# Optimization experiments

Hardware: AMD Instinct MI355X
Metric: run time of the kernel (lower is better)

The kernel has to match this reference:

```python
import jax, jax.numpy as jnp
import numpy as np
import math

B = 2        # batch
S = 4095     # input sequence (cls token makes L = 4096)
F_IN = 32    # input feature size
D = 512      # d_model (hidden_size)
H = 8        # n_heads
E = D // H   # head dim = 64
DFF = 2048   # feedforward dim
NL = 2       # encoder layers
FACTOR = 5   # probsparse sampling factor
EPS = 1e-5


def setup_inputs() -> dict:
    key = jax.random.key(0)
    ks = jax.random.split(key, 16)

    def w(k, shape):
        return jax.random.normal(k, shape, dtype=jnp.float32) * 0.02

    inp = {}
    inp['x'] = jax.random.normal(ks[0], (B, S, F_IN), dtype=jnp.float32)
    inp['We'] = w(ks[1], (D, F_IN)); inp['be'] = jnp.zeros((D,), jnp.float32)
    inp['cls'] = jnp.zeros((1, 1, D), jnp.float32)
    inp['Wq'] = w(ks[2], (NL, D, D)); inp['bq'] = jnp.zeros((NL, D), jnp.float32)
    inp['Wk'] = w(ks[3], (NL, D, D)); inp['bk'] = jnp.zeros((NL, D), jnp.float32)
    inp['Wv'] = w(ks[4], (NL, D, D)); inp['bv'] = jnp.zeros((NL, D), jnp.float32)
    inp['Wo'] = w(ks[5], (NL, D, D)); inp['bo'] = jnp.zeros((NL, D), jnp.float32)
    inp['g1'] = jnp.ones((NL, D), jnp.float32); inp['b1'] = jnp.zeros((NL, D), jnp.float32)
    inp['g2'] = jnp.ones((NL, D), jnp.float32); inp['b2'] = jnp.zeros((NL, D), jnp.float32)
    inp['W1'] = w(ks[6], (NL, DFF, D)); inp['bf1'] = jnp.zeros((NL, DFF), jnp.float32)
    inp['W2'] = w(ks[7], (NL, D, DFF)); inp['bf2'] = jnp.zeros((NL, D), jnp.float32)
    inp['Wf'] = w(ks[8], (1, D)); inp['bf'] = jnp.zeros((1,), jnp.float32)
    return inp


def pos_encoding(L):
    # Sinusoidal positional encoding [L, D]
    pos = jnp.arange(L, dtype=jnp.float32)[:, None]
    div = jnp.exp(jnp.arange(0, D, 2, dtype=jnp.float32) * (-math.log(10000.0) / D))
    pe = jnp.zeros((L, D), jnp.float32)
    pe = pe.at[:, 0::2].set(jnp.sin(pos * div))
    pe = pe.at[:, 1::2].set(jnp.cos(pos * div))
    return pe


def layer_norm(x, g, b):
    mu = x.mean(-1, keepdims=True)
    var = ((x - mu) ** 2).mean(-1, keepdims=True)
    return (x - mu) / jnp.sqrt(var + EPS) * g + b


def prob_attention(q, k, v, rng):
    # q, k, v: [B, H, L, E]; mask_flag=False (encoder self-attention)
    b, h, L, e = q.shape
    u = min(FACTOR * int(np.ceil(np.log(L))), L)  # sample_k == n_top here (L_Q == L_K)
    idx = jax.random.randint(rng, (L, u), 0, L)   # random K sampling per query position
    Ks = k[:, :, idx, :]                          # [B,H,L,u,E] gather
    QKs = jnp.einsum('bhle,bhlue->bhlu', q, Ks)   # sampled scores
    M = QKs.max(-1) - QKs.sum(-1) / L             # sparsity measure [B,H,L]
    _, top = jax.lax.top_k(M, u)                  # active query indices [B,H,u]
    Qr = jnp.take_along_axis(q, top[..., None], axis=2)      # [B,H,u,E]
    scores = jnp.einsum('bhue,bhke->bhuk', Qr, k) / math.sqrt(e)
    attn = jax.nn.softmax(scores, axis=-1)
    ctx = jnp.broadcast_to(v.mean(axis=2, keepdims=True), (b, h, L, e))  # initial context = mean(V)
    upd = jnp.einsum('bhuk,bhke->bhue', attn, v)
    bi = jnp.arange(b)[:, None, None]
    hi = jnp.arange(h)[None, :, None]
    ctx = ctx.at[bi, hi, top].set(upd)            # scatter active-query contexts
    return ctx                                    # [B,H,L,E]


def attention_layer(x, Wq_, bq_, Wk_, bk_, Wv_, bv_, Wo_, bo_, rng):
    b, L, _ = x.shape
    q = (x @ Wq_.T + bq_).reshape(b, L, H, E).transpose(0, 2, 1, 3)
    k = (x @ Wk_.T + bk_).reshape(b, L, H, E).transpose(0, 2, 1, 3)
    v = (x @ Wv_.T + bv_).reshape(b, L, H, E).transpose(0, 2, 1, 3)
    ctx = prob_attention(q, k, v, rng)            # [B,H,L,E]
    out = ctx.transpose(0, 2, 1, 3).reshape(b, L, D)
    return out @ Wo_.T + bo_


def reference(x, We, be, cls, Wq, bq, Wk, bk, Wv, bv, Wo, bo, g1, b1, g2, b2, W1, bf1, W2, bf2, Wf, bf):
    h = x @ We.T + be                                            # [B,S,D]
    h = jnp.concatenate([jnp.broadcast_to(cls, (B, 1, D)), h], axis=1)  # prepend cls
    L = h.shape[1]
    h = h + pos_encoding(L)[None]
    for l in range(NL):
        rng = jax.random.fold_in(jax.random.key(42), l)
        a = attention_layer(h, Wq[l], bq[l], Wk[l], bk[l], Wv[l], bv[l], Wo[l], bo[l], rng)
        h = layer_norm(h + a, g1[l], b1[l])
        y = jax.nn.relu(h @ W1[l].T + bf1[l])
        y = y @ W2[l].T + bf2[l]
        h = layer_norm(h + y, g2[l], b2[l])
    return h[:, 0] @ Wf.T + bf  # cls-token prediction head [B,1]
```

## Files before the change

kernel.cpp:

```cpp
#include <hip/hip_runtime.h>
#include <hip/hip_bf16.h>
#include <math.h>
#include <stdint.h>

#define B 2
#define S 4095
#define LSEQ 4096
#define F_IN 32
#define D 512
#define H 8
#define E 64
#define DFF 2048
#define NL 2
#define U 45
#define EPSL 1e-5f
#define LU (LSEQ * U)
#define HALF_LU (LU / 2)
#define NS 32
#define SLICE 128

typedef __attribute__((ext_vector_type(8))) short short8;
typedef __attribute__((ext_vector_type(4))) float f32x4;

#define GLD(gp, lp)                                                            \
    __builtin_amdgcn_global_load_lds(                                          \
        (const __attribute__((address_space(1))) void*)(gp),                   \
        (__attribute__((address_space(3))) void*)(lp), 16, 0, 0)

__device__ __forceinline__ unsigned short bf16_bits(float f) {
    __hip_bfloat16 h = __float2bfloat16(f);
    return *(unsigned short*)&h;
}
__device__ __forceinline__ float bits_to_f32(unsigned short s) {
    union { uint32_t u; float f; } c;
    c.u = ((uint32_t)s) << 16;
    return c.f;
}
__device__ __forceinline__ unsigned long long mkey(float v, int index) {
    uint32_t u = __float_as_uint(v);
    uint32_t mono = (u & 0x80000000u) ? ~u : (u | 0x80000000u);
    return ((unsigned long long)mono << 32) | (uint32_t)(0xFFFFFFFFu - (uint32_t)index);
}

__device__ __forceinline__ uint32_t rotl32(uint32_t x, int r) {
    return (x << r) | (x >> (32 - r));
}

__device__ void threefry2x32(uint32_t k0, uint32_t k1, uint32_t c0, uint32_t c1,
                             uint32_t& o0, uint32_t& o1) {
    uint32_t ks2 = k0 ^ k1 ^ 0x1BD11BDAu;
    uint32_t x0 = c0 + k0, x1 = c1 + k1;
    x0 += x1; x1 = rotl32(x1, 13); x1 ^= x0;
    x0 += x1; x1 = rotl32(x1, 15); x1 ^= x0;
    x0 += x1; x1 = rotl32(x1, 26); x1 ^= x0;
    x0 += x1; x1 = rotl32(x1, 6);  x1 ^= x0;
    x0 += k1; x1 += ks2 + 1u;
    x0 += x1; x1 = rotl32(x1, 17); x1 ^= x0;
    x0 += x1; x1 = rotl32(x1, 29); x1 ^= x0;
    x0 += x1; x1 = rotl32(x1, 16); x1 ^= x0;
    x0 += x1; x1 = rotl32(x1, 24); x1 ^= x0;
    x0 += ks2; x1 += k0 + 2u;
    x0 += x1; x1 = rotl32(x1, 13); x1 ^= x0;
    x0 += x1; x1 = rotl32(x1, 15); x1 ^= x0;
    x0 += x1; x1 = rotl32(x1, 26); x1 ^= x0;
    x0 += x1; x1 = rotl32(x1, 6);  x1 ^= x0;
    x0 += k0; x1 += k1 + 3u;
    x0 += x1; x1 = rotl32(x1, 17); x1 ^= x0;
    x0 += x1; x1 = rotl32(x1, 29); x1 ^= x0;
    x0 += x1; x1 = rotl32(x1, 16); x1 ^= x0;
    x0 += x1; x1 = rotl32(x1, 24); x1 ^= x0;
    x0 += k1; x1 += ks2 + 4u;
    x0 += x1; x1 = rotl32(x1, 13); x1 ^= x0;
    x0 += x1; x1 = rotl32(x1, 15); x1 ^= x0;
    x0 += x1; x1 = rotl32(x1, 26); x1 ^= x0;
    x0 += x1; x1 = rotl32(x1, 6);  x1 ^= x0;
    x0 += ks2; x1 += k0 + 5u;
    o0 = x0; o1 = x1;
}

__global__ void idx_kernel(int* __restrict__ idx, int layer) {
    int j = blockIdx.x * blockDim.x + threadIdx.x;
    if (j >= HALF_LU) return;
    uint32_t f0, f1, a0, a1, b0, b1, o0, o1;
    threefry2x32(0u, 42u, 0u, (uint32_t)layer, f0, f1);
    threefry2x32(f0, f1, 0u, 2u, a0, a1);
    threefry2x32(f0, f1, 1u, 3u, b0, b1);
    threefry2x32(a1, b1, (uint32_t)j, (uint32_t)(j + HALF_LU), o0, o1);
    idx[j] = (int)(o0 & 4095u);
    idx[j + HALF_LU] = (int)(o1 & 4095u);
    (void)a0; (void)b0;
}

__global__ void prep_embed_kernel(const float* __restrict__ x, const float* __restrict__ We,
                                  __hip_bfloat16* __restrict__ xbf,
                                  __hip_bfloat16* __restrict__ webf) {
    int u = blockIdx.x * blockDim.x + threadIdx.x;
    const int NX = B * LSEQ * F_IN / 4;
    const int NW = D * F_IN / 4;
    if (u < NX) {
        int e0 = u * 4;
        int i = e0 & 31;
        int l = (e0 >> 5) & (LSEQ - 1);
        int b = e0 >> 17;
        union { unsigned short s[4]; uint2 w; } o;
        if (l == 0) {
            o.s[0] = o.s[1] = o.s[2] = o.s[3] = 0;
        } else {
            float4 v = *(const float4*)(x + ((size_t)b * S + (l - 1)) * F_IN + i);
            o.s[0] = bf16_bits(v.x); o.s[1] = bf16_bits(v.y);
            o.s[2] = bf16_bits(v.z); o.s[3] = bf16_bits(v.w);
        }
        ((uint2*)xbf)[u] = o.w;
    } else if (u < NX + NW) {
        int w = u - NX;
        float4 v = ((const float4*)We)[w];
        union { unsigned short s[4]; uint2 w2; } o;
        o.s[0] = bf16_bits(v.x); o.s[1] = bf16_bits(v.y);
        o.s[2] = bf16_bits(v.z); o.s[3] = bf16_bits(v.w);
        ((uint2*)webf)[w] = o.w2;
    }
}

__global__ void posenc_kernel(const float* __restrict__ emb, const float* __restrict__ cls,
                              float* __restrict__ h, __hip_bfloat16* __restrict__ hbf) {
    int gid = blockIdx.x * blockDim.x + threadIdx.x;
    if (gid >= B * LSEQ * D) return;
    int d = gid % D;
    int l = (gid / D) % LSEQ;
    float v = (l == 0) ? cls[d] : emb[gid];
    int i = d >> 1;
    float divv = expf((float)(2 * i) * (float)(-9.210340371976184 / 512.0));
    float ang = (float)l * divv;
    v += (d & 1) ? cosf(ang) : sinf(ang);
    h[gid] = v;
    hbf[gid] = __float2bfloat16(v);
}

__global__ void cast_weights_kernel(const float* __restrict__ Wq_l,
                                    const float* __restrict__ Wk_l,
                                    const float* __restrict__ Wv_l,
                                    const float* __restrict__ Wo_l,
                                    const float* __restrict__ W1_l,
                                    const float* __restrict__ W2_l,
                                    const float* __restrict__ bq_l,
                                    const float* __restrict__ bk_l,
                                    const float* __restrict__ bv_l,
                                    __hip_bfloat16* __restrict__ wqb,
                                    __hip_bfloat16* __restrict__ wkb,
                                    __hip_bfloat16* __restrict__ wvb,
                                    __hip_bfloat16* __restrict__ wob,
                                    __hip_bfloat16* __restrict__ w1b,
                                    __hip_bfloat16* __restrict__ w2b,
                                    float* __restrict__ qkvbias) {
    const int SDD = D * D / 4;
    const int SFD = DFF * D / 4;
    const int CAST_N = 4 * SDD + 2 * SFD;
    int u = blockIdx.x * blockDim.x + threadIdx.x;
    if (u >= CAST_N) {
        int j = u - CAST_N;
        if (j < 384) {
            int seg = (j * 4) >> 9;
            int off = (j * 4) & 511;
            const float* src = (seg == 0) ? bq_l : (seg == 1) ? bk_l : bv_l;
            *(float4*)(qkvbias + j * 4) = *(const float4*)(src + off);
        }
        return;
    }
    const float* src;
    __hip_bfloat16* dst;
    int off;
    if (u < SDD) { src = Wq_l; dst = wqb; off = u; }
    else if (u < 2 * SDD) { src = Wk_l; dst = wkb; off = u - SDD; }
    else if (u < 3 * SDD) { src = Wv_l; dst = wvb; off = u - 2 * SDD; }
    else if (u < 4 * SDD) { src = Wo_l; dst = wob; off = u - 3 * SDD; }
    else if (u < 4 * SDD + SFD) { src = W1_l; dst = w1b; off = u - 4 * SDD; }
    else { src = W2_l; dst = w2b; off = u - 4 * SDD - SFD; }
    float4 v = ((const float4*)src)[off];
    union { unsigned short s[4]; uint2 w; } o;
    o.s[0] = bf16_bits(v.x); o.s[1] = bf16_bits(v.y);
    o.s[2] = bf16_bits(v.z); o.s[3] = bf16_bits(v.w);
    ((uint2*)dst)[off] = o.w;
}

__global__ __launch_bounds__(256) void gemm32(const unsigned short* __restrict__ A,
                                              const unsigned short* __restrict__ W,
                                              const float* __restrict__ bias,
                                              float* __restrict__ Cf,
                                              int M, int N, int K) {
    __shared__ unsigned short lds[2 * 128 * 32];
    unsigned short* As = lds;
    unsigned short* Bs = lds + 128 * 32;
    const int tid = threadIdx.x;
    const int m0 = blockIdx.y * 128, n0 = blockIdx.x * 128;
    const int wave = tid >> 6, lane = tid & 63;
    const int wm = (wave >> 1) * 64, wn = (wave & 1) * 64;
    const int quad = lane >> 4, m15 = lane & 15;
    const int srow = tid >> 2, scol = (tid & 3) * 8;
    f32x4 acc[4][4] = {};
    const unsigned short* Ag0 = A + (size_t)(m0 + srow) * K + scol;
    const unsigned short* Ag1 = A + (size_t)(m0 + srow + 64) * K + scol;
    const unsigned short* Wg0 = W + (size_t)(n0 + srow) * K + scol;
    const unsigned short* Wg1 = W + (size_t)(n0 + srow + 64) * K + scol;
    for (int k0 = 0; k0 < K; k0 += 32) {
        __syncthreads();
        GLD(Ag0 + k0, As + tid * 8);
        GLD(Ag1 + k0, As + 2048 + tid * 8);
        GLD(Wg0 + k0, Bs + tid * 8);
        GLD(Wg1 + k0, Bs + 2048 + tid * 8);
        __syncthreads();
        short8 af[4], bfr[4];
#pragma unroll
        for (int mi = 0; mi < 4; ++mi)
            af[mi] = *(const short8*)(As + (wm + mi * 16 + m15) * 32 + quad * 8);
#pragma unroll
        for (int ni = 0; ni < 4; ++ni)
            bfr[ni] = *(const short8*)(Bs + (wn + ni * 16 + m15) * 32 + quad * 8);
#pragma unroll
        for (int mi = 0; mi < 4; ++mi)
#pragma unroll
            for (int ni = 0; ni < 4; ++ni)
                acc[mi][ni] = __builtin_amdgcn_mfma_f32_16x16x32_bf16(
                    af[mi], bfr[ni], acc[mi][ni], 0, 0, 0);
    }
#pragma unroll
    for (int mi = 0; mi < 4; ++mi) {
        int mg = m0 + wm + mi * 16 + quad * 4;
#pragma unroll
        for (int ni = 0; ni < 4; ++ni) {
            int ng = n0 + wn + ni * 16 + m15;
            float bv = bias[ng];
#pragma unroll
            for (int r = 0; r < 4; ++r)
                Cf[(size_t)(mg + r) * N + ng] = acc[mi][ni][r] + bv;
        }
    }
}

template <int MODE>
__global__ __launch_bounds__(256) void gemm_pipe(const unsigned short* __restrict__ A,
                                                 const unsigned short* __restrict__ W,
                                                 const float* __restrict__ bias,
                                                 void* __restrict__ C0,
                                                 void* __restrict__ C1,
                                                 void* __restrict__ C2,
                                                 int M, int N, int K, int NBN) {
    __shared__ unsigned short As[2][128 * 32];
    __shared__ unsigned short Bs[2][128 * 32];
    const int tid = threadIdx.x;
    const int NBM = M >> 7;
    const int bid = blockIdx.x;
    const int xcd = bid & 7, local = bid >> 3;
    const int m_t = xcd * (NBM >> 3) + local / NBN;
    const int n_t = local % NBN;
    const int m0 = m_t * 128, n0 = n_t * 128;
    const int wave = tid >> 6, lane = tid & 63;
    const int wm = (wave >> 1) * 64, wn = (wave & 1) * 64;
    const int quad = lane >> 4, m15 = lane & 15;
    const int srow = tid >> 2, scol = (tid & 3) * 8;
    f32x4 acc[4][4] = {};
    const unsigned short* Ag0 = A + (size_t)(m0 + srow) * K + scol;
    const unsigned short* Ag1 = A + (size_t)(m0 + srow + 64) * K + scol;
    const unsigned short* Wg0 = W + (size_t)(n0 + srow) * K + scol;
    const unsigned short* Wg1 = W + (size_t)(n0 + srow + 64) * K + scol;
    GLD(Ag0, As[0] + tid * 8);
    GLD(Ag1, As[0] + 2048 + tid * 8);
    GLD(Wg0, Bs[0] + tid * 8);
    GLD(Wg1, Bs[0] + 2048 + tid * 8);
    int cur = 0;
    for (int k0 = 0; k0 < K; k0 += 32) {
        __syncthreads();
        int kn = k0 + 32;
        if (kn < K) {
            GLD(Ag0 + kn, As[cur ^ 1] + tid * 8);
            GLD(Ag1 + kn, As[cur ^ 1] + 2048 + tid * 8);
            GLD(Wg0 + kn, Bs[cur ^ 1] + tid * 8);
            GLD(Wg1 + kn, Bs[cur ^ 1] + 2048 + tid * 8);
        }
        short8 af[4], bfr[4];
#pragma unroll
        for (int mi = 0; mi < 4; ++mi)
            af[mi] = *(const short8*)(As[cur] + (wm + mi * 16 + m15) * 32 + quad * 8);
#pragma unroll
        for (int ni = 0; ni < 4; ++ni)
            bfr[ni] = *(const short8*)(Bs[cur] + (wn + ni * 16 + m15) * 32 + quad * 8);
#pragma unroll
        for (int mi = 0; mi < 4; ++mi)
#pragma unroll
            for (int ni = 0; ni < 4; ++ni)
                acc[mi][ni] = __builtin_amdgcn_mfma_f32_16x16x32_bf16(
                    af[mi], bfr[ni], acc[mi][ni], 0, 0, 0);
        cur ^= 1;
    }
#pragma unroll
    for (int mi = 0; mi < 4; ++mi) {
        int mg = m0 + wm + mi * 16 + quad * 4;
#pragma unroll
        for (int ni = 0; ni < 4; ++ni) {
            int ng = n0 + wn + ni * 16 + m15;
            float bv = bias[ng];
#pragma unroll
            for (int r = 0; r < 4; ++r) {
                float v = acc[mi][ni][r] + bv;
                if (MODE == 0) {
                    ((float*)C0)[(size_t)(mg + r) * N + ng] = v;
                } else if (MODE == 1) {
                    ((__hip_bfloat16*)C0)[(size_t)(mg + r) * N + ng] = __float2bfloat16(v);
                } else if (MODE == 2) {
                    ((__hip_bfloat16*)C0)[(size_t)(mg + r) * N + ng] =
                        __float2bfloat16(fmaxf(v, 0.f));
                } else {
                    int seg = ng >> 9;
                    int col = ng & 511;
                    if (seg == 0)
                        ((float*)C0)[(size_t)(mg + r) * D + col] = v;
                    else if (seg == 1)
                        ((__hip_bfloat16*)C1)[(size_t)(mg + r) * D + col] = __float2bfloat16(v);
                    else
                        ((__hip_bfloat16*)C2)[(size_t)(mg + r) * D + col] = __float2bfloat16(v);
                }
            }
        }
    }
}

__global__ __launch_bounds__(256) void gemm64_m64(const unsigned short* __restrict__ A,
                                                  const unsigned short* __restrict__ W,
                                                  const float* __restrict__ bias,
                                                  float* __restrict__ Cf,
                                                  int M, int N, int K, int NBN) {
    __shared__ unsigned short As[2][64 * 32];
    __shared__ unsigned short Bs[2][128 * 32];
    const int tid = threadIdx.x;
    const int NBM = M >> 6;
    const int bid = blockIdx.x;
    const int xcd = bid & 7, local = bid >> 3;
    const int m_t = xcd * (NBM >> 3) + local / NBN;
    const int n_t = local % NBN;
    const int m0 = m_t * 64, n0 = n_t * 128;
    const int wave = tid >> 6, lane = tid & 63;
    const int quad = lane >> 4, m15 = lane & 15;
    const int srow = tid >> 2, scol = (tid & 3) * 8;
    f32x4 acc[8] = {};
    const unsigned short* Ag0 = A + (size_t)(m0 + srow) * K + scol;
    const unsigned short* Wg0 = W + (size_t)(n0 + srow) * K + scol;
    const unsigned short* Wg1 = W + (size_t)(n0 + srow + 64) * K + scol;
    for (int k0 = 0; k0 < K; k0 += 64) {
        __syncthreads();
        if (tid * 8 < 64 * 32) {
            GLD(Ag0 + k0, As[0] + tid * 8);
            GLD(Ag0 + k0 + 32, As[1] + tid * 8);
        }
        GLD(Wg0 + k0, Bs[0] + tid * 8);
        GLD(Wg1 + k0, Bs[0] + 2048 + tid * 8);
        GLD(Wg0 + k0 + 32, Bs[1] + tid * 8);
        GLD(Wg1 + k0 + 32, Bs[1] + 2048 + tid * 8);
        __syncthreads();
#pragma unroll
        for (int ks = 0; ks < 2; ++ks) {
            short8 af = *(const short8*)(As[ks] + (wave * 16 + m15) * 32 + quad * 8);
#pragma unroll
            for (int ni = 0; ni < 8; ++ni) {
                short8 bfr = *(const short8*)(Bs[ks] + (ni * 16 + m15) * 32 + quad * 8);
                acc[ni] = __builtin_amdgcn_mfma_f32_16x16x32_bf16(af, bfr, acc[ni], 0, 0, 0);
            }
        }
    }
    int mg = m0 + wave * 16 + quad * 4;
#pragma unroll
    for (int ni = 0; ni < 8; ++ni) {
        int ng = n0 + ni * 16 + m15;
        float bv = bias[ng];
#pragma unroll
        for (int r = 0; r < 4; ++r)
            Cf[(size_t)(mg + r) * N + ng] = acc[ni][r] + bv;
    }
}

__global__ __launch_bounds__(256) void mscore_kernel(const float* __restrict__ q,
                                                     const __hip_bfloat16* __restrict__ kbf,
                                                     const int* __restrict__ idx,
                                                     float* __restrict__ Mv) {
    __shared__ float Sbuf[U][8];
    __shared__ int sidx[U];
    int bid = blockIdx.x;
    int b = bid & 1;
    int l = bid >> 1;
    int tid = threadIdx.x;
    int wave = tid >> 6, lane = tid & 63;
    if (tid < U) sidx[tid] = idx[l * U + tid];
    const float* qr = q + ((size_t)(b * LSEQ) + l) * D + lane * 8;
    float4 qa = *(const float4*)qr;
    float4 qb = *(const float4*)(qr + 4);
    __syncthreads();
    const unsigned short* kbase = (const unsigned short*)(kbf + (size_t)(b * LSEQ) * D);
    for (int t = wave; t < U; t += 4) {
        int kr = sidx[t];
        union { uint4 u; unsigned short s[8]; } kv;
        kv.u = *(const uint4*)(kbase + (size_t)kr * D + lane * 8);
        float p = qa.x * bits_to_f32(kv.s[0]) + qa.y * bits_to_f32(kv.s[1]) +
                  qa.z * bits_to_f32(kv.s[2]) + qa.w * bits_to_f32(kv.s[3]) +
                  qb.x * bits_to_f32(kv.s[4]) + qb.y * bits_to_f32(kv.s[5]) +
                  qb.z * bits_to_f32(kv.s[6]) + qb.w * bits_to_f32(kv.s[7]);
        p += __shfl_xor(p, 1);
        p += __shfl_xor(p, 2);
        p += __shfl_xor(p, 4);
        if ((lane & 7) == 0) Sbuf[t][lane >> 3] = p;
    }
    __syncthreads();
    if (tid < 8) {
        float mx = -INFINITY, sm = 0.f;
        for (int t = 0; t < U; ++t) {
            float v = Sbuf[t][tid];
            mx = fmaxf(mx, v);
            sm += v;
        }
        Mv[((size_t)b * H + tid) * LSEQ + l] = mx - sm / (float)LSEQ;
    }
}

__global__ __launch_bounds__(256) void topk_chunk_kernel(const float* __restrict__ Mv,
                                                         unsigned long long* __restrict__ cand) {
    __shared__ unsigned long long sk[256];
    int blk = blockIdx.x;
    int chunk = blk & 15, bh = blk >> 4;
    int tid = threadIdx.x;
    int gi = chunk * 256 + tid;
    sk[tid] = mkey(Mv[(size_t)bh * LSEQ + gi], gi);
    __syncthreads();
    for (int k = 2; k <= 256; k <<= 1) {
        for (int j = k >> 1; j > 0; j >>= 1) {
            int ixj = tid ^ j;
            if (ixj > tid) {
                unsigned long long a = sk[tid], b = sk[ixj];
                bool desc = ((tid & k) == 0);
                if (desc ? (a < b) : (a > b)) { sk[tid] = b; sk[ixj] = a; }
            }
            __syncthreads();
        }
    }
    if (tid < U) cand[((size_t)bh * 16 + chunk) * U + tid] = sk[tid];
}

__global__ __launch_bounds__(256) void topk_merge_kernel(const unsigned long long* __restrict__ cand,
                                                         int* __restrict__ top) {
    __shared__ unsigned long long sk[1024];
    int bh = blockIdx.x;
    int tid = threadIdx.x;
    for (int e = tid; e < 1024; e += 256)
        sk[e] = (e < 16 * U) ? cand[(size_t)bh * 16 * U + e] : 0ull;
    __syncthreads();
    for (int k = 2; k <= 1024; k <<= 1) {
        for (int j = k >> 1; j > 0; j >>= 1) {
            for (int e = tid; e < 1024; e += 256) {
                int ixj = e ^ j;
                if (ixj > e) {
                    unsigned long long a = sk[e], b = sk[ixj];
                    bool desc = ((e & k) == 0);
                    if (desc ? (a < b) : (a > b)) { sk[e] = b; sk[ixj] = a; }
                }
            }
            __syncthreads();
        }
    }
    if (tid < U)
        top[bh * U + tid] = (int)(0xFFFFFFFFu - (uint32_t)(sk[tid] & 0xFFFFFFFFu));
}

__global__ __launch_bounds__(256) void vmean_part(const __hip_bfloat16* __restrict__ v,
                                                  float* __restrict__ part) {
    int blk = blockIdx.x;
    int seg = blk & 7, hh = (blk >> 3) & 7, b = blk >> 6;
    int e = threadIdx.x & 63, rg = threadIdx.x >> 6;
    const __hip_bfloat16* vp =
        v + ((size_t)(b * LSEQ) + seg * 512) * D + hh * 64 + e;
    float acc = 0.f;
    for (int r = rg; r < 512; r += 4) acc += __bfloat162float(vp[(size_t)r * D]);
    __shared__ float red[4][64];
    red[rg][e] = acc;
    __syncthreads();
    if (threadIdx.x < 64)
        part[(size_t)blk * 64 + threadIdx.x] =
            red[0][threadIdx.x] + red[1][threadIdx.x] + red[2][threadIdx.x] + red[3][threadIdx.x];
}

__global__ void vmean_reduce(const float* __restrict__ part, float* __restrict__ vm) {
    int gid = blockIdx.x * blockDim.x + threadIdx.x;
    if (gid >= B * H * E) return;
    int e = gid & 63, bh = gid >> 6;
    float acc = 0.f;
#pragma unroll
    for (int s = 0; s < 8; ++s) acc += part[((size_t)bh * 8 + s) * 64 + e];
    vm[gid] = acc / (float)LSEQ;
}

__global__ __launch_bounds__(256) void wo_base_kernel(const float* __restrict__ vm,
                                                      const unsigned short* __restrict__ wob,
                                                      const float* __restrict__ bo,
                                                      float* __restrict__ base) {
    int b = blockIdx.x >> 7;
    int n = (blockIdx.x & 127) * 4 + (threadIdx.x >> 6);
    int lane = threadIdx.x & 63;
    const float* vmr = vm + (size_t)b * D + lane * 8;
    float4 va = *(const float4*)vmr;
    float4 vb = *(const float4*)(vmr + 4);
    union { uint4 u; unsigned short s[8]; } w;
    w.u = *(const uint4*)(wob + (size_t)n * D + lane * 8);
    float p = va.x * bits_to_f32(w.s[0]) + va.y * bits_to_f32(w.s[1]) +
              va.z * bits_to_f32(w.s[2]) + va.w * bits_to_f32(w.s[3]) +
              vb.x * bits_to_f32(w.s[4]) + vb.y * bits_to_f32(w.s[5]) +
              vb.z * bits_to_f32(w.s[6]) + vb.w * bits_to_f32(w.s[7]);
    for (int off = 32; off; off >>= 1) p += __shfl_xor(p, off);
    if (lane == 0) base[(size_t)b * D + n] = p + bo[n];
}

__global__ void bcast_base(const float* __restrict__ base, float* __restrict__ aout) {
    int i = blockIdx.x * blockDim.x + threadIdx.x;
    if (i >= B * LSEQ * D / 4) return;
    int b = i >> 19;
    int c4 = i & 127;
    ((float4*)aout)[i] = *(const float4*)(base + (size_t)b * D + c4 * 4);
}

__global__ __launch_bounds__(256) void wo_corr_kernel(const float* __restrict__ updbuf,
                                                      const float* __restrict__ vm,
                                                      const unsigned short* __restrict__ wob,
                                                      const int* __restrict__ top,
                                                      float* __restrict__ aout) {
    __shared__ float dlt[E];
    int bid = blockIdx.x;
    int t = bid % U;
    int bh = bid / U;
    int b = bh >> 3, hh = bh & 7;
    int tid = threadIdx.x;
    if (tid < E) dlt[tid] = updbuf[((size_t)bh * U + t) * E + tid] - vm[(size_t)bh * E + tid];
    __syncthreads();
    int r = top[bh * U + t];
    float* arow = aout + (size_t)(b * LSEQ + r) * D;
    for (int n = tid; n < D; n += 256) {
        const unsigned short* wr = wob + (size_t)n * D + hh * E;
        float acc = 0.f;
#pragma unroll
        for (int k2 = 0; k2 < E; ++k2) acc += dlt[k2] * bits_to_f32(wr[k2]);
        atomicAdd(arow + n, acc);
    }
}

__global__ __launch_bounds__(256) void attn_part(const float* __restrict__ q,
                                                 const __hip_bfloat16* __restrict__ kbf,
                                                 const __hip_bfloat16* __restrict__ vbf,
                                                 const int* __restrict__ top,
                                                 float* __restrict__ Opart,
                                                 float* __restrict__ msum) {
    __shared__ unsigned short Qs[48 * 72];
    __shared__ unsigned short Ks[SLICE * 72];
    __shared__ unsigned short Vs[SLICE * 68];
    __shared__ unsigned short Ps[48 * 136];
    __shared__ float mred[48][4];
    __shared__ float sred[48][4];
    const int slice = blockIdx.x, hh = blockIdx.y, b = blockIdx.z;
    const int bh = b * H + hh;
    const int tid = threadIdx.x;
    const int s0 = slice * SLICE;
    for (int i = tid; i < 48 * 64; i += 256) {
        int t = i >> 6, e = i & 63;
        float v = 0.f;
        if (t < U) {
            int r = top[bh * U + t];
            v = q[((size_t)(b * LSEQ) + r) * D + hh * E + e];
        }
        Qs[t * 72 + e] = bf16_bits(v);
    }
    {
        const uint4* src = (const uint4*)(kbf + ((size_t)(b * LSEQ) + s0) * D + hh * E);
        for (int i = tid; i < SLICE * 8; i += 256) {
            int r = i >> 3, c = i & 7;
            uint4 d = src[(size_t)r * 64 + c];
            *(uint4*)(Ks + r * 72 + c * 8) = d;
        }
    }
    {
        const uint2* src = (const uint2*)(vbf + ((size_t)(b * LSEQ) + s0) * D + hh * E);
        for (int i = tid; i < SLICE * 16; i += 256) {
            int r = i >> 4, c = i & 15;
            uint2 d = src[(size_t)r * 128 + c];
            *(uint2*)(Vs + r * 68 + c * 4) = d;
        }
    }
    __syncthreads();
    const int wave = tid >> 6, lane = tid & 63;
    const int quad = lane >> 4, m15 = lane & 15;
    const int wc = wave * 32;
    f32x4 acc[3][2] = {};
#pragma unroll
    for (int ks = 0; ks < 2; ++ks) {
        short8 af[3], bfr[2];
#pragma unroll
        for (int mt = 0; mt < 3; ++mt)
            af[mt] = *(const short8*)(Qs + (mt * 16 + m15) * 72 + ks * 32 + quad * 8);
#pragma unroll
        for (int nt = 0; nt < 2; ++nt)
            bfr[nt] = *(const short8*)(Ks + (wc + nt * 16 + m15) * 72 + ks * 32 + quad * 8);
#pragma unroll
        for (int mt = 0; mt < 3; ++mt)
#pragma unroll
            for (int nt = 0; nt < 2; ++nt)
                acc[mt][nt] = __builtin_amdgcn_mfma_f32_16x16x32_bf16(
                    af[mt], bfr[nt], acc[mt][nt], 0, 0, 0);
    }
    float sc[3][2][4];
#pragma unroll
    for (int mt = 0; mt < 3; ++mt)
#pragma unroll
        for (int nt = 0; nt < 2; ++nt)
#pragma unroll
            for (int r = 0; r < 4; ++r) sc[mt][nt][r] = acc[mt][nt][r] * 0.125f;
#pragma unroll
    for (int mt = 0; mt < 3; ++mt)
#pragma unroll
        for (int r = 0; r < 4; ++r) {
            float mv = fmaxf(sc[mt][0][r], sc[mt][1][r]);
            mv = fmaxf(mv, __shfl_xor(mv, 1));
            mv = fmaxf(mv, __shfl_xor(mv, 2));
            mv = fmaxf(mv, __shfl_xor(mv, 4));
            mv = fmaxf(mv, __shfl_xor(mv, 8));
            if (m15 == 0) mred[mt * 16 + quad * 4 + r][wave] = mv;
        }
    __syncthreads();
#pragma unroll
    for (int mt = 0; mt < 3; ++mt)
#pragma unroll
        for (int r = 0; r < 4; ++r) {
            int row = mt * 16 + quad * 4 + r;
            float ms = fmaxf(fmaxf(mred[row][0], mred[row][1]),
                             fmaxf(mred[row][2], mred[row][3]));
            float p0 = __expf(sc[mt][0][r] - ms);
            float p1 = __expf(sc[mt][1][r] - ms);
            float sv = p0 + p1;
            sv += __shfl_xor(sv, 1);
            sv += __shfl_xor(sv, 2);
            sv += __shfl_xor(sv, 4);
            sv += __shfl_xor(sv, 8);
            if (m15 == 0) sred[row][wave] = sv;
            Ps[row * 136 + wc + m15] = bf16_bits(p0);
            Ps[row * 136 + wc + 16 + m15] = bf16_bits(p1);
        }
    __syncthreads();
    if (tid < U) {
        float mm = fmaxf(fmaxf(mred[tid][0], mred[tid][1]),
                         fmaxf(mred[tid][2], mred[tid][3]));
        float ss = sred[tid][0] + sred[tid][1] + sred[tid][2] + sred[tid][3];
        size_t base = (((size_t)bh * NS + slice) * U + tid) * 2;
        msum[base] = mm;
        msum[base + 1] = ss;
    }
    f32x4 apv[3] = {};
#pragma unroll
    for (int ks = 0; ks < 4; ++ks) {
        short8 bv;
#pragma unroll
        for (int j = 0; j < 8; ++j)
            bv[j] = (short)Vs[(ks * 32 + quad * 8 + j) * 68 + wave * 16 + m15];
        short8 af2[3];
#pragma unroll
        for (int mt = 0; mt < 3; ++mt)
            af2[mt] = *(const short8*)(Ps + (mt * 16 + m15) * 136 + ks * 32 + quad * 8);
#pragma unroll
        for (int mt = 0; mt < 3; ++mt)
            apv[mt] = __builtin_amdgcn_mfma_f32_16x16x32_bf16(af2[mt], bv, apv[mt], 0, 0, 0);
    }
    size_t obase = ((size_t)bh * NS + slice) * U;
#pragma unroll
    for (int mt = 0; mt < 3; ++mt)
#pragma unroll
        for (int r = 0; r < 4; ++r) {
            int row = mt * 16 + quad * 4 + r;
            if (row < U)
                Opart[(obase + row) * 64 + wave * 16 + m15] = apv[mt][r];
        }
}

__global__ __launch_bounds__(64) void attn_reduce(const float* __restrict__ Opart,
                                                  const float* __restrict__ msum,
                                                  float* __restrict__ updbuf) {
    int t = blockIdx.x % U;
    int bh = blockIdx.x / U;
    int lane = threadIdx.x;
    float m_s = -INFINITY, ss = 0.f;
    if (lane < NS) {
        size_t base = (((size_t)bh * NS + lane) * U + t) * 2;
        m_s = msum[base];
        ss = msum[base + 1];
    }
    float M = m_s;
    for (int off = 32; off; off >>= 1) M = fmaxf(M, __shfl_xor(M, off));
    float e_s = (lane < NS) ? __expf(m_s - M) : 0.f;
    float d = ss * e_s;
    for (int off = 32; off; off >>= 1) d += __shfl_xor(d, off);
    float acc = 0.f;
    for (int s = 0; s < NS; ++s) {
        float w = __shfl(e_s, s);
        acc += w * Opart[(((size_t)bh * NS + s) * U + t) * 64 + lane];
    }
    updbuf[((size_t)bh * U + t) * E + lane] = acc / d;
}

__global__ __launch_bounds__(64) void add_ln_kernel(float* __restrict__ h,
                                                    const float* __restrict__ a,
                                                    const float* __restrict__ g,
                                                    const float* __restrict__ bb,
                                                    __hip_bfloat16* __restrict__ hbf) {
    int row = blockIdx.x;
    int lane = threadIdx.x;
    float* hp = h + (size_t)row * D;
    const float* ap = a + (size_t)row * D;
    float x[8];
    float sum = 0.f;
#pragma unroll
    for (int j = 0; j < 8; ++j) {
        x[j] = hp[lane + 64 * j] + ap[lane + 64 * j];
        sum += x[j];
    }
    for (int off = 32; off; off >>= 1) sum += __shfl_xor(sum, off);
    float mu = sum / (float)D;
    float vs = 0.f;
#pragma unroll
    for (int j = 0; j < 8; ++j) {
        float dd = x[j] - mu;
        vs += dd * dd;
    }
    for (int off = 32; off; off >>= 1) vs += __shfl_xor(vs, off);
    float inv = 1.f / sqrtf(vs / (float)D + EPSL);
#pragma unroll
    for (int j = 0; j < 8; ++j) {
        float o = (x[j] - mu) * inv * g[lane + 64 * j] + bb[lane + 64 * j];
        hp[lane + 64 * j] = o;
        hbf[(size_t)row * D + lane + 64 * j] = __float2bfloat16(o);
    }
}

__global__ void final_kernel(const float* __restrict__ h, const float* __restrict__ Wf,
                             const float* __restrict__ bf, float* __restrict__ out) {
    int b = blockIdx.x;
    int lane = threadIdx.x;
    const float* hp = h + (size_t)b * LSEQ * D;
    float acc = 0.f;
    for (int j = lane; j < D; j += 64) acc += hp[j] * Wf[j];
    for (int off = 32; off; off >>= 1) acc += __shfl_xor(acc, off);
    if (lane == 0) out[b] = acc + bf[0];
}

extern "C" void kernel_launch(void* const* d_in, const int* in_sizes, int n_in,
                              void* d_out, int out_size, void* d_ws, size_t ws_size,
                              hipStream_t stream) {
    (void)in_sizes; (void)n_in; (void)out_size; (void)ws_size;
    const float* x   = (const float*)d_in[0];
    const float* We  = (const float*)d_in[1];
    const float* be  = (const float*)d_in[2];
    const float* cls = (const float*)d_in[3];
    const float* Wq  = (const float*)d_in[4];
    const float* bq  = (const float*)d_in[5];
    const float* Wk  = (const float*)d_in[6];
    const float* bk  = (const float*)d_in[7];
    const float* Wv  = (const float*)d_in[8];
    const float* bv  = (const float*)d_in[9];
    const float* Wo  = (const float*)d_in[10];
    const float* bo  = (const float*)d_in[11];
    const float* g1  = (const float*)d_in[12];
    const float* b1  = (const float*)d_in[13];
    const float* g2  = (const float*)d_in[14];
    const float* b2  = (const float*)d_in[15];
    const float* W1  = (const float*)d_in[16];
    const float* bf1 = (const float*)d_in[17];
    const float* W2  = (const float*)d_in[18];
    const float* bf2 = (const float*)d_in[19];
    const float* Wf  = (const float*)d_in[20];
    const float* bff = (const float*)d_in[21];
    float* out = (float*)d_out;

    float* ws = (float*)d_ws;
    const size_t NT = (size_t)B * LSEQ * D;
    float* h    = ws;
    float* aout = ws + NT;
    float* q    = ws + 2 * NT;
    __hip_bfloat16* kbf    = (__hip_bfloat16*)(ws + NT);
    __hip_bfloat16* y1_bf  = (__hip_bfloat16*)(ws + 2 * NT);
    __hip_bfloat16* v_bf   = (__hip_bfloat16*)(ws + 4 * NT);
    __hip_bfloat16* h_bf   = (__hip_bfloat16*)(ws + 5 * NT);
    float* Opart = ws + 3 * NT;
    float* msumb = Opart + (size_t)B * H * NS * U * 64;
    float* wpool = ws + 5 * NT + NT / 2;
    __hip_bfloat16* wqb = (__hip_bfloat16*)wpool;
    __hip_bfloat16* wkb = wqb + (size_t)D * D;
    __hip_bfloat16* wvb = wkb + (size_t)D * D;
    __hip_bfloat16* wob = wvb + (size_t)D * D;
    __hip_bfloat16* w1b = wob + (size_t)D * D;
    __hip_bfloat16* w2b = w1b + (size_t)DFF * D;
    float* after_w = wpool + ((size_t)4 * D * D + 2 * (size_t)DFF * D) / 2;
    float* Mbuf = after_w;
    int* idx    = (int*)(Mbuf + (size_t)B * H * LSEQ);
    int* top    = idx + LU;
    float* vm   = (float*)(top + B * H * U);
    float* vpart  = vm + (size_t)B * H * E;
    float* updbuf = vpart + (size_t)128 * 64;
    float* baseb  = updbuf + (size_t)B * H * U * 64;
    __hip_bfloat16* xbf  = (__hip_bfloat16*)(baseb + (size_t)B * D);
    __hip_bfloat16* webf = xbf + (size_t)B * LSEQ * F_IN;
    unsigned long long* cand =
        (unsigned long long*)(((uintptr_t)(webf + (size_t)D * F_IN) + 7) & ~(uintptr_t)7);
    float* qkvbias = (float*)(cand + (size_t)B * H * 16 * U);

    const int ML = B * LSEQ;
    dim3 gD(D / 128, ML / 128);
    const int CAST_N = 4 * (D * D / 4) + 2 * (DFF * D / 4);
    const int CAST_TOT = CAST_N + 384;

    prep_embed_kernel<<<(B * LSEQ * F_IN / 4 + D * F_IN / 4 + 255) / 256, 256, 0, stream>>>(
        x, We, xbf, webf);
    gemm32<<<gD, 256, 0, stream>>>((const unsigned short*)xbf,
                                   (const unsigned short*)webf, be, aout, ML, D, F_IN);
    posenc_kernel<<<(B * LSEQ * D + 255) / 256, 256, 0, stream>>>(aout, cls, h, h_bf);

    for (int l = 0; l < NL; ++l) {
        cast_weights_kernel<<<(CAST_TOT + 255) / 256, 256, 0, stream>>>(
            Wq + (size_t)l * D * D, Wk + (size_t)l * D * D, Wv + (size_t)l * D * D,
            Wo + (size_t)l * D * D, W1 + (size_t)l * DFF * D, W2 + (size_t)l * D * DFF,
            bq + l * D, bk + l * D, bv + l * D,
            wqb, wkb, wvb, wob, w1b, w2b, qkvbias);

        gemm_pipe<3><<<768, 256, 0, stream>>>((const unsigned short*)h_bf,
                                              (const unsigned short*)wqb, qkvbias,
                                              q, kbf, v_bf, ML, 3 * D, D, 12);

        idx_kernel<<<(HALF_LU + 255) / 256, 256, 0, stream>>>(idx, l);
        mscore_kernel<<<B * LSEQ, 256, 0, stream>>>(q, kbf, idx, Mbuf);
        topk_chunk_kernel<<<B * H * 16, 256, 0, stream>>>(Mbuf, cand);
        topk_merge_kernel<<<B * H, 256, 0, stream>>>(cand, top);
        vmean_part<<<B * H * 8, 256, 0, stream>>>(v_bf, vpart);
        vmean_reduce<<<4, 256, 0, stream>>>(vpart, vm);
        wo_base_kernel<<<B * 128, 256, 0, stream>>>(vm, (const unsigned short*)wob,
                                                    bo + l * D, baseb);
        attn_part<<<dim3(NS, H, B), 256, 0, stream>>>(q, kbf, v_bf, top, Opart, msumb);
        attn_reduce<<<B * H * U, 64, 0, stream>>>(Opart, msumb, updbuf);
        bcast_base<<<(B * LSEQ * D / 4 + 255) / 256, 256, 0, stream>>>(baseb, aout);
        wo_corr_kernel<<<B * H * U, 256, 0, stream>>>(updbuf, vm,
                                                      (const unsigned short*)wob, top, aout);
        add_ln_kernel<<<ML, 64, 0, stream>>>(h, aout, g1 + l * D, b1 + l * D, h_bf);

        gemm_pipe<2><<<1024, 256, 0, stream>>>((const unsigned short*)h_bf,
                                               (const unsigned short*)w1b, bf1 + l * DFF,
                                               y1_bf, nullptr, nullptr, ML, DFF, D, 16);
        gemm64_m64<<<512, 256, 0, stream>>>((const unsigned short*)y1_bf,
                                            (const unsigned short*)w2b, bf2 + l * D,
                                            aout, ML, D, DFF, 4);
        add_ln_kernel<<<ML, 64, 0, stream>>>(h, aout, g2 + l * D, b2 + l * D, h_bf);
    }

    final_kernel<<<B, 64, 0, stream>>>(h, Wf, bff, out);
}
```

Baseline: 664.4 us.

## Replace broadcast of attention base with sparse correction rows and flags

Stops writing the broadcast base output to every row of the full [B,L,D] buffer. Only the top-query rows are zeroed and marked in a per-row flag array, the per-query attention reduction is fused into the Wo correction kernel, and the layer-norm kernel adds the per-batch base plus the correction only for flagged rows. This removes a full-size write and read of the attention output and one launch. It adds a flag buffer that is cleared inside the weight-cast kernel and a small extra zeroing kernel.

```diff
diff --git a/kernel.cpp b/kernel.cpp
--- a/kernel.cpp
+++ b/kernel.cpp
@@ -151,7 +151,8 @@
                                     __hip_bfloat16* __restrict__ wob,
                                     __hip_bfloat16* __restrict__ w1b,
                                     __hip_bfloat16* __restrict__ w2b,
-                                    float* __restrict__ qkvbias) {
+                                    float* __restrict__ qkvbias,
+                                    unsigned char* __restrict__ flags) {
     const int SDD = D * D / 4;
     const int SFD = DFF * D / 4;
     const int CAST_N = 4 * SDD + 2 * SFD;
@@ -163,6 +164,8 @@
             int off = (j * 4) & 511;
             const float* src = (seg == 0) ? bq_l : (seg == 1) ? bk_l : bv_l;
             *(float4*)(qkvbias + j * 4) = *(const float4*)(src + off);
+        } else if (j < 384 + B * LSEQ / 4) {
+            ((int*)flags)[j - 384] = 0;
         }
         return;
     }
@@ -513,26 +516,52 @@
     if (lane == 0) base[(size_t)b * D + n] = p + bo[n];
 }
 
-__global__ void bcast_base(const float* __restrict__ base, float* __restrict__ aout) {
-    int i = blockIdx.x * blockDim.x + threadIdx.x;
-    if (i >= B * LSEQ * D / 4) return;
-    int b = i >> 19;
-    int c4 = i & 127;
-    ((float4*)aout)[i] = *(const float4*)(base + (size_t)b * D + c4 * 4);
-}
-
-__global__ __launch_bounds__(256) void wo_corr_kernel(const float* __restrict__ updbuf,
-                                                      const float* __restrict__ vm,
-                                                      const unsigned short* __restrict__ wob,
-                                                      const int* __restrict__ top,
-                                                      float* __restrict__ aout) {
+__global__ __launch_bounds__(128) void zero_corr_kernel(const int* __restrict__ top,
+                                                        float* __restrict__ aout,
+                                                        unsigned char* __restrict__ flags) {
+    int bid = blockIdx.x;
+    int t = bid % U;
+    int bh = bid / U;
+    int b = bh >> 3;
+    int r = top[bh * U + t];
+    int tid = threadIdx.x;
+    float4 z = {0.f, 0.f, 0.f, 0.f};
+    ((float4*)(aout + (size_t)(b * LSEQ + r) * D))[tid] = z;
+    if (tid == 0) flags[b * LSEQ + r] = 1;
+}
+
+__global__ __launch_bounds__(256) void attnred_corr_kernel(const float* __restrict__ Opart,
+                                                           const float* __restrict__ msum,
+                                                           const float* __restrict__ vm,
+                                                           const unsigned short* __restrict__ wob,
+                                                           const int* __restrict__ top,
+                                                           float* __restrict__ aout) {
     __shared__ float dlt[E];
     int bid = blockIdx.x;
     int t = bid % U;
     int bh = bid / U;
     int b = bh >> 3, hh = bh & 7;
     int tid = threadIdx.x;
-    if (tid < E) dlt[tid] = updbuf[((size_t)bh * U + t) * E + tid] - vm[(size_t)bh * E + tid];
+    if (tid < 64) {
+        int lane = tid;
+        float m_s = -INFINITY, ss = 0.f;
+        if (lane < NS) {
+            size_t base = (((size_t)bh * NS + lane) * U + t) * 2;
+            m_s = msum[base];
+            ss = msum[base + 1];
+        }
+        float M = m_s;
+        for (int off = 32; off; off >>= 1) M = fmaxf(M, __shfl_xor(M, off));
+        float e_s = (lane < NS) ? __expf(m_s - M) : 0.f;
+        float d = ss * e_s;
+        for (int off = 32; off; off >>= 1) d += __shfl_xor(d, off);
+        float acc = 0.f;
+        for (int s = 0; s < NS; ++s) {
+            float w = __shfl(e_s, s);
+            acc += w * Opart[(((size_t)bh * NS + s) * U + t) * 64 + lane];
+        }
+        dlt[lane] = acc / d - vm[(size_t)bh * E + lane];
+    }
     __syncthreads();
     int r = top[bh * U + t];
     float* arow = aout + (size_t)(b * LSEQ + r) * D;
@@ -679,29 +708,45 @@
         }
 }
 
-__global__ __launch_bounds__(64) void attn_reduce(const float* __restrict__ Opart,
-                                                  const float* __restrict__ msum,
-                                                  float* __restrict__ updbuf) {
-    int t = blockIdx.x % U;
-    int bh = blockIdx.x / U;
+__global__ __launch_bounds__(64) void add_ln_base_kernel(float* __restrict__ h,
+                                                         const float* __restrict__ base,
+                                                         const float* __restrict__ aout,
+                                                         const unsigned char* __restrict__ flags,
+                                                         const float* __restrict__ g,
+                                                         const float* __restrict__ bb,
+                                                         __hip_bfloat16* __restrict__ hbf) {
+    int row = blockIdx.x;
+    int b = row >> 12;
     int lane = threadIdx.x;
-    float m_s = -INFINITY, ss = 0.f;
-    if (lane < NS) {
-        size_t base = (((size_t)bh * NS + lane) * U + t) * 2;
-        m_s = msum[base];
-        ss = msum[base + 1];
-    }
-    float M = m_s;
-    for (int off = 32; off; off >>= 1) M = fmaxf(M, __shfl_xor(M, off));
-    float e_s = (lane < NS) ? __expf(m_s - M) : 0.f;
-    float d = ss * e_s;
-    for (int off = 32; off; off >>= 1) d += __shfl_xor(d, off);
-    float acc = 0.f;
-    for (int s = 0; s < NS; ++s) {
-        float w = __shfl(e_s, s);
-        acc += w * Opart[(((size_t)bh * NS + s) * U + t) * 64 + lane];
-    }
-    updbuf[((size_t)bh * U + t) * E + lane] = acc / d;
+    float* hp = h + (size_t)row * D;
+    const float* bp = base + (size_t)b * D;
+    const float* ap = aout + (size_t)row * D;
+    bool has = flags[row] != 0;
+    float x[8];
+    float sum = 0.f;
+#pragma unroll
+    for (int j = 0; j < 8; ++j) {
+        float a = bp[lane + 64 * j];
+        if (has) a += ap[lane + 64 * j];
+        x[j] = hp[lane + 64 * j] + a;
+        sum += x[j];
+    }
+    for (int off = 32; off; off >>= 1) sum += __shfl_xor(sum, off);
+    float mu = sum / (float)D;
+    float vs = 0.f;
+#pragma unroll
+    for (int j = 0; j < 8; ++j) {
+        float dd = x[j] - mu;
+        vs += dd * dd;
+    }
+    for (int off = 32; off; off >>= 1) vs += __shfl_xor(vs, off);
+    float inv = 1.f / sqrtf(vs / (float)D + EPSL);
+#pragma unroll
+    for (int j = 0; j < 8; ++j) {
+        float o = (x[j] - mu) * inv * g[lane + 64 * j] + bb[lane + 64 * j];
+        hp[lane + 64 * j] = o;
+        hbf[(size_t)row * D + lane + 64 * j] = __float2bfloat16(o);
+    }
 }
 
 __global__ __launch_bounds__(64) void add_ln_kernel(float* __restrict__ h,
@@ -801,18 +846,18 @@
     int* top    = idx + LU;
     float* vm   = (float*)(top + B * H * U);
     float* vpart  = vm + (size_t)B * H * E;
-    float* updbuf = vpart + (size_t)128 * 64;
-    float* baseb  = updbuf + (size_t)B * H * U * 64;
+    float* baseb  = vpart + (size_t)128 * 64;
     __hip_bfloat16* xbf  = (__hip_bfloat16*)(baseb + (size_t)B * D);
     __hip_bfloat16* webf = xbf + (size_t)B * LSEQ * F_IN;
     unsigned long long* cand =
         (unsigned long long*)(((uintptr_t)(webf + (size_t)D * F_IN) + 7) & ~(uintptr_t)7);
     float* qkvbias = (float*)(cand + (size_t)B * H * 16 * U);
+    unsigned char* flags = (unsigned char*)(qkvbias + 1536);
 
     const int ML = B * LSEQ;
     dim3 gD(D / 128, ML / 128);
     const int CAST_N = 4 * (D * D / 4) + 2 * (DFF * D / 4);
-    const int CAST_TOT = CAST_N + 384;
+    const int CAST_TOT = CAST_N + 384 + B * LSEQ / 4;
 
     prep_embed_kernel<<<(B * LSEQ * F_IN / 4 + D * F_IN / 4 + 255) / 256, 256, 0, stream>>>(
         x, We, xbf, webf);
@@ -825,7 +870,7 @@
             Wq + (size_t)l * D * D, Wk + (size_t)l * D * D, Wv + (size_t)l * D * D,
             Wo + (size_t)l * D * D, W1 + (size_t)l * DFF * D, W2 + (size_t)l * D * DFF,
             bq + l * D, bk + l * D, bv + l * D,
-            wqb, wkb, wvb, wob, w1b, w2b, qkvbias);
+            wqb, wkb, wvb, wob, w1b, w2b, qkvbias, flags);
 
         gemm_pipe<3><<<768, 256, 0, stream>>>((const unsigned short*)h_bf,
                                               (const unsigned short*)wqb, qkvbias,
@@ -840,11 +885,12 @@
         wo_base_kernel<<<B * 128, 256, 0, stream>>>(vm, (const unsigned short*)wob,
                                                     bo + l * D, baseb);
         attn_part<<<dim3(NS, H, B), 256, 0, stream>>>(q, kbf, v_bf, top, Opart, msumb);
-        attn_reduce<<<B * H * U, 64, 0, stream>>>(Opart, msumb, updbuf);
-        bcast_base<<<(B * LSEQ * D / 4 + 255) / 256, 256, 0, stream>>>(baseb, aout);
-        wo_corr_kernel<<<B * H * U, 256, 0, stream>>>(updbuf, vm,
-                                                      (const unsigned short*)wob, top, aout);
-        add_ln_kernel<<<ML, 64, 0, stream>>>(h, aout, g1 + l * D, b1 + l * D, h_bf);
+        zero_corr_kernel<<<B * H * U, 128, 0, stream>>>(top, aout, flags);
+        attnred_corr_kernel<<<B * H * U, 256, 0, stream>>>(Opart, msumb, vm,
+                                                           (const unsigned short*)wob, top,
+                                                           aout);
+        add_ln_base_kernel<<<ML, 64, 0, stream>>>(h, baseb, aout, flags,
+                                                  g1 + l * D, b1 + l * D, h_bf);
 
         gemm_pipe<2><<<1024, 256, 0, stream>>>((const unsigned short*)h_bf,
                                                (const unsigned short*)w1b, bf1 + l * DFF,
```

New measurement: 651.8 us. About the same (-1.9%).
